# Kernel optimization log

Hardware: AMD Instinct MI355X
Metric: run time of the kernel (lower is better)

## Reference

```python
import jax, jax.numpy as jnp
import numpy as np

R, C, H, W = 500, 512, 38, 38      # rois, VGG channels, feature-map HxW (img 608 / 16)
K, HID, POOL, SCALE = 20, 4096, 3, 16
FEAT = C * POOL * POOL             # 4608, matches fc6 in_features


def setup_inputs():
    key = jax.random.key(0)
    ks = jax.random.split(key, 12)
    fmap = jax.random.normal(ks[0], (C, H, W), dtype=jnp.float32)
    # ROIs in original image coords (x1,y1,x2,y2); width/height >= 48 px so that
    # after /16 + floor every ROI is non-degenerate (none filtered out).
    x1 = jax.random.randint(ks[1], (R,), 0, 288)
    y1 = jax.random.randint(ks[2], (R,), 0, 288)
    bw = jax.random.randint(ks[3], (R,), 48, 304)
    bh = jax.random.randint(ks[4], (R,), 48, 304)
    rois = jnp.stack([x1, y1, x1 + bw, y1 + bh], axis=1).astype(jnp.float32)
    label = jax.random.bernoulli(ks[5], 0.3, (K,)).astype(jnp.float32)
    s = 0.01
    W6 = jax.random.normal(ks[6], (FEAT, HID), jnp.float32) * s
    b6 = jnp.zeros((HID,), jnp.float32)
    W7 = jax.random.normal(ks[7], (HID, HID), jnp.float32) * s
    b7 = jnp.zeros((HID,), jnp.float32)
    W8c = jax.random.normal(ks[8], (HID, K), jnp.float32) * s
    b8c = jnp.zeros((K,), jnp.float32)
    W8d = jax.random.normal(ks[9], (HID, K), jnp.float32) * s
    b8d = jnp.zeros((K,), jnp.float32)
    return dict(fmap=fmap, rois=rois, label=label, W6=W6, b6=b6, W7=W7, b7=b7,
                W8c=W8c, b8c=b8c, W8d=W8d, b8d=b8d)


def _roi_pool(fmap, rois):
    # scaled_rois = origin_rois / 16, sliced as integer indices (floor)
    sc = jnp.floor(rois / SCALE).astype(jnp.int32)          # [R,4]
    x1, y1, x2, y2 = sc[:, 0], sc[:, 1], sc[:, 2], sc[:, 3]

    def binmask(lo, hi, size):
        # adaptive-max-pool bins: [lo + floor(j*L/3), lo + ceil((j+1)*L/3))
        L = hi - lo                                          # [R]
        j = jnp.arange(POOL)
        start = lo[:, None] + (j[None, :] * L[:, None]) // POOL
        end = lo[:, None] + (-((-(j[None, :] + 1) * L[:, None]) // POOL))
        pos = jnp.arange(size)
        return (pos[None, None, :] >= start[:, :, None]) & (pos[None, None, :] < end[:, :, None])

    cm = binmask(x1, x2, W)                                  # [R,3,W]
    rm = binmask(y1, y2, H)                                  # [R,3,H]
    neg = jnp.finfo(fmap.dtype).min
    # max over x within each x-bin: [R,C,H,3]
    tmp = jnp.max(jnp.where(cm[:, None, None, :, :], fmap[None, :, :, None, :], neg), axis=-1)
    # max over y within each y-bin: [R,C,3,3]
    pooled = jnp.max(jnp.where(rm[:, None, :, :, None], tmp[:, :, None, :, :], neg), axis=3)
    return pooled.reshape(R, FEAT), sc.astype(jnp.float32)


def _spatial_reg(scores, fc7, rois_sc, label):
    # faithful to original: argsort ascending, index 0 taken as the reference box,
    # and bboxes_iou interprets (x1,y1,x2,y2) as (x,y,w,h) — replicated as-is.
    idx = jnp.argsort(scores, axis=0)                        # [R,K]

    def per_class(idx_k, s_k, lab_k):
        h, rest = idx_k[0], idx_k[1:]
        hb = rois_sc[h]                                      # [4]
        rb = rois_sc[rest]                                   # [R-1,4]
        b1x2, b1y2 = rb[:, 0] + rb[:, 2], rb[:, 1] + rb[:, 3]
        b2x2, b2y2 = hb[0] + hb[2], hb[1] + hb[3]
        iw = jnp.clip(jnp.minimum(b1x2, b2x2) - jnp.maximum(rb[:, 0], hb[0]) + 1, 0)
        ih = jnp.clip(jnp.minimum(b1y2, b2y2) - jnp.maximum(rb[:, 1], hb[1]) + 1, 0)
        inter = iw * ih
        a1 = (b1x2 - rb[:, 0] + 1) * (b1y2 - rb[:, 1] + 1)
        a2 = (b2x2 - hb[0] + 1) * (b2y2 - hb[1] + 1)
        iou = inter / (a1 + a2 - inter)
        m = (iou > 0.6).astype(fc7.dtype)                    # [R-1]
        rf = fc7[rest] * m[:, None]
        diff = (rf - fc7[h]) * s_k[rest][:, None]
        return lab_k * 0.5 * jnp.sum(diff * diff)

    regs = jax.vmap(per_class)(idx.T, scores.T, label)       # [K]
    return jnp.sum(regs) / K


def reference(fmap, rois, label, W6, b6, W7, b7, W8c, b8c, W8d, b8d):
    feat, rois_sc = _roi_pool(fmap, rois)                    # [R,4608]
    fc6 = feat @ W6 + b6
    fc7 = fc6 @ W7 + b7
    pc = jax.nn.softmax(fc7 @ W8c + b8c, axis=1)             # per-roi over classes
    pd = jax.nn.softmax(fc7 @ W8d + b8d, axis=0)             # per-class over rois
    scores = pc * pd                                         # [R,K]
    out = jnp.sum(scores, axis=0)                            # [K], in (0,1)
    bce = -jnp.mean(label * jnp.log(out) + (1.0 - label) * jnp.log(1.0 - out))
    reg = _spatial_reg(scores, fc7, rois_sc, label)
    return scores, bce + reg, reg
```

## Files before the change

kernel.cpp:

```cpp
#include <hip/hip_runtime.h>
#include <cstdint>
#include <cstddef>

#define DEV __device__ __forceinline__

typedef __bf16 bf16_t;
typedef __bf16 bf16x8 __attribute__((ext_vector_type(8)));
typedef float  f32x4  __attribute__((ext_vector_type(4)));
typedef float  f32x2  __attribute__((ext_vector_type(2)));
typedef unsigned int u32x4 __attribute__((ext_vector_type(4)));

DEV bf16_t f2bf(float x) { return (bf16_t)x; }

constexpr int R_ = 500, C_ = 512, H_ = 38, W_ = 38, K_ = 20;
constexpr int HID = 4096, FEAT = 4608, MP = 512;
constexpr int HW = H_ * W_;

constexpr size_t alup(size_t x) { return (x + 255) & ~(size_t)255; }
constexpr size_t O_FMT  = 0;
constexpr size_t O_RSC  = alup(O_FMT  + (size_t)HW*C_*4);
constexpr size_t O_FEAT = alup(O_RSC  + (size_t)R_*4*4);
constexpr size_t O_FC6  = alup(O_FEAT + (size_t)MP*FEAT*2);
constexpr size_t O_FC7  = alup(O_FC6  + (size_t)MP*HID*2);
constexpr size_t O_PC   = alup(O_FC7  + (size_t)MP*HID*4);
constexpr size_t O_LD   = alup(O_PC   + (size_t)R_*K_*4);
constexpr size_t O_AN   = alup(O_LD   + (size_t)R_*K_*4);
constexpr size_t O_OS   = alup(O_AN   + (size_t)MP*4);
constexpr size_t O_HI   = alup(O_OS   + (size_t)K_*4);
constexpr size_t O_D    = alup(O_HI   + (size_t)K_*4);
constexpr size_t O_W8T  = alup(O_D    + (size_t)R_*K_*4);
constexpr size_t O_PART = alup(O_W8T  + (size_t)2*K_*HID*4);
constexpr size_t WS_K4  = O_PART + (size_t)4*MP*HID*4;

__global__ void __launch_bounds__(256) k_transpose(const float* __restrict__ fmap,
                                                   float* __restrict__ fmapt) {
    __shared__ float tile[32][33];
    int p0 = blockIdx.x * 32, c0 = blockIdx.y * 32;
    int tx = threadIdx.x & 31, ty = threadIdx.x >> 5;
#pragma unroll
    for (int i = 0; i < 4; ++i) {
        int c = c0 + ty + i*8, p = p0 + tx;
        tile[ty + i*8][tx] = (p < HW) ? fmap[(size_t)c*HW + p] : 0.f;
    }
    __syncthreads();
#pragma unroll
    for (int i = 0; i < 4; ++i) {
        int p = p0 + ty + i*8, c = c0 + tx;
        if (p < HW) fmapt[(size_t)p*C_ + c] = tile[tx][ty + i*8];
    }
}

__global__ void __launch_bounds__(256) k_w8t(const float* __restrict__ W8c,
                                             const float* __restrict__ W8d,
                                             float* __restrict__ W8T) {
    int k = blockIdx.x;
    const float* src = (k < K_) ? W8c : W8d;
    int kk = (k < K_) ? k : k - K_;
    for (int i = threadIdx.x; i < HID; i += 256)
        W8T[(size_t)k*HID + i] = src[(size_t)i*K_ + kk];
}

__global__ void __launch_bounds__(256) k_roipool(const float* __restrict__ fmapt,
                                                 const float* __restrict__ rois,
                                                 bf16_t* __restrict__ feat,
                                                 float* __restrict__ rois_sc) {
    int r = blockIdx.x, bin = blockIdx.y, t = threadIdx.x;
    if (r >= R_) {
        feat[(size_t)r*FEAT + (size_t)t*9       + bin] = (bf16_t)0.f;
        feat[(size_t)r*FEAT + (size_t)(t+256)*9 + bin] = (bf16_t)0.f;
        return;
    }
    int x1 = (int)floorf(rois[r*4+0] * 0.0625f);
    int y1 = (int)floorf(rois[r*4+1] * 0.0625f);
    int x2 = (int)floorf(rois[r*4+2] * 0.0625f);
    int y2 = (int)floorf(rois[r*4+3] * 0.0625f);
    if (bin == 0 && t == 0) {
        rois_sc[r*4+0] = (float)x1; rois_sc[r*4+1] = (float)y1;
        rois_sc[r*4+2] = (float)x2; rois_sc[r*4+3] = (float)y2;
    }
    int Lx = x2 - x1, Ly = y2 - y1;
    int pr = bin / 3, px = bin - pr*3;
    int rs = y1 + (pr*Ly)/3, re = y1 + ((pr+1)*Ly + 2)/3;
    int cs = x1 + (px*Lx)/3, ce = x1 + ((px+1)*Lx + 2)/3;
    float m0 = -3.402823466e38f, m1 = -3.402823466e38f;
    for (int y = rs; y < re; ++y) {
        const float* rowp = fmapt + (size_t)(y*W_)*C_;
        for (int x = cs; x < ce; ++x) {
            const float* p = rowp + (size_t)x*C_;
            m0 = fmaxf(m0, p[t]);
            m1 = fmaxf(m1, p[t + 256]);
        }
    }
    feat[(size_t)r*FEAT + (size_t)t*9       + bin] = f2bf(m0);
    feat[(size_t)r*FEAT + (size_t)(t+256)*9 + bin] = f2bf(m1);
}

__global__ void __launch_bounds__(256, 2)
k_gemm(const bf16_t* __restrict__ A, const float* __restrict__ B,
       float* __restrict__ part, int KDIM, int nts) {
    __shared__ bf16_t Asm[2][128*64];
    __shared__ bf16_t Bsm[2][128*64];
    const int t = threadIdx.x;
    const int lane = t & 63, wid = t >> 6;
    const int wr = wid >> 1, wc = wid & 1;

    const int flat = blockIdx.x + 32*blockIdx.y + 128*blockIdx.z;
    const int q = 16 * gridDim.z;
    const int v = (flat & 7) * q + (flat >> 3);
    const int by = v & 3, bx = (v >> 2) & 31, bz = v >> 7;

    const int brow = by * 128, bcol = bx * 128;
    const int kt0 = bz * nts;

    f32x4 acc[4][4] = {};
    f32x2 br[16];
    const int n2 = t & 63, kgl = t >> 6;

    auto stage_A = [&](int kt, int buf) {
        const bf16_t* Ag = A + (size_t)brow*KDIM + kt*64;
#pragma unroll
        for (int i = 0; i < 4; ++i) {
            int s = t + i*256;
            int row = s >> 3;
            int kb = (s & 7) ^ ((row >> 1) & 7);
            const bf16_t* src = Ag + (size_t)row*KDIM + kb*8;
            bf16_t* dst = &Asm[buf][(size_t)(i*256 + (t & ~63)) * 8];
            __builtin_amdgcn_global_load_lds(
                (const __attribute__((address_space(1))) void*)src,
                (__attribute__((address_space(3))) void*)dst, 16, 0, 0);
        }
    };
    auto load_B = [&](int kt) {
        const float* src = B + (size_t)(kt*64 + kgl*16)*HID + bcol + 2*n2;
#pragma unroll
        for (int j = 0; j < 16; ++j)
            br[j] = *reinterpret_cast<const f32x2*>(src + (size_t)j*HID);
    };
    auto write_B = [&](int buf) {
        const int sw = n2 & 7;
        bf16x8 v0, v1;
#pragma unroll
        for (int j = 0; j < 8; ++j) { v0[j] = f2bf(br[j].x); v1[j] = f2bf(br[j+8].x); }
        *reinterpret_cast<u32x4*>(&Bsm[buf][(size_t)((2*n2)*8 + ((kgl*2    ) ^ sw)) * 8]) = *reinterpret_cast<u32x4*>(&v0);
        *reinterpret_cast<u32x4*>(&Bsm[buf][(size_t)((2*n2)*8 + ((kgl*2 + 1) ^ sw)) * 8]) = *reinterpret_cast<u32x4*>(&v1);
#pragma unroll
        for (int j = 0; j < 8; ++j) { v0[j] = f2bf(br[j].y); v1[j] = f2bf(br[j+8].y); }
        *reinterpret_cast<u32x4*>(&Bsm[buf][(size_t)((2*n2+1)*8 + ((kgl*2    ) ^ sw)) * 8]) = *reinterpret_cast<u32x4*>(&v0);
        *reinterpret_cast<u32x4*>(&Bsm[buf][(size_t)((2*n2+1)*8 + ((kgl*2 + 1) ^ sw)) * 8]) = *reinterpret_cast<u32x4*>(&v1);
    };

    stage_A(kt0, 0);
    load_B(kt0);
    write_B(0);
    __syncthreads();

    for (int it = 0; it < nts; ++it) {
        const int cur = it & 1;
        if (it + 1 < nts) { stage_A(kt0 + it + 1, cur ^ 1); load_B(kt0 + it + 1); }
#pragma unroll
        for (int kk = 0; kk < 2; ++kk) {
            const int kb = kk*4 + (lane >> 4);
            bf16x8 af[4], bfr[4];
#pragma unroll
            for (int m = 0; m < 4; ++m) {
                int row = wr*64 + m*16 + (lane & 15);
                af[m] = *reinterpret_cast<const bf16x8*>(
                    &Asm[cur][(size_t)(row*8 + (kb ^ ((row >> 1) & 7))) * 8]);
            }
#pragma unroll
            for (int n = 0; n < 4; ++n) {
                int nn = wc*64 + n*16 + (lane & 15);
                bfr[n] = *reinterpret_cast<const bf16x8*>(
                    &Bsm[cur][(size_t)(nn*8 + (kb ^ ((nn >> 1) & 7))) * 8]);
            }
#pragma unroll
            for (int m = 0; m < 4; ++m)
#pragma unroll
                for (int n = 0; n < 4; ++n)
                    acc[m][n] = __builtin_amdgcn_mfma_f32_16x16x32_bf16(af[m], bfr[n], acc[m][n], 0, 0, 0);
        }
        if (it + 1 < nts) { write_B(cur ^ 1); __syncthreads(); }
    }

    float* dst = part + (size_t)bz * MP * HID;
#pragma unroll
    for (int m = 0; m < 4; ++m) {
        int row0 = brow + wr*64 + m*16 + ((lane >> 4) << 2);
#pragma unroll
        for (int n = 0; n < 4; ++n) {
            int col = bcol + wc*64 + n*16 + (lane & 15);
#pragma unroll
            for (int j = 0; j < 4; ++j)
                dst[(size_t)(row0 + j)*HID + col] = acc[m][n][j];
        }
    }
}

__global__ void __launch_bounds__(256) k_reduce(const float* __restrict__ part,
                                                const float* __restrict__ bias,
                                                bf16_t* __restrict__ ob, float* __restrict__ of,
                                                int ksplit) {
    size_t idx = ((size_t)blockIdx.x*256 + threadIdx.x) * 4;
    f32x4 s = *reinterpret_cast<const f32x4*>(part + idx);
    for (int ss = 1; ss < ksplit; ++ss)
        s += *reinterpret_cast<const f32x4*>(part + (size_t)ss*MP*HID + idx);
    int col = (int)(idx & (HID - 1));
    s += *reinterpret_cast<const f32x4*>(bias + col);
    if (ob) {
#pragma unroll
        for (int j = 0; j < 4; ++j) ob[idx + j] = f2bf(s[j]);
    } else {
        *reinterpret_cast<f32x4*>(of + idx) = s;
    }
}

__global__ void __launch_bounds__(256) k_heads(const float* __restrict__ fc7,
        const float* __restrict__ W8T,
        const float* __restrict__ b8c, const float* __restrict__ b8d,
        float* __restrict__ pc, float* __restrict__ ld_out, float* __restrict__ An) {
    int r = blockIdx.x, t = threadIdx.x;
    float ac[20] = {}, ad[20] = {}, aa = 0.f;
    const float* frow = fc7 + (size_t)r*HID;
    for (int e = 0; e < 16; ++e) {
        int i = e*256 + t;
        float x = frow[i];
        aa = fmaf(x, x, aa);
#pragma unroll
        for (int k = 0; k < 20; ++k) {
            ac[k] = fmaf(x, W8T[(size_t)k*HID + i], ac[k]);
            ad[k] = fmaf(x, W8T[(size_t)(K_ + k)*HID + i], ad[k]);
        }
    }
#pragma unroll
    for (int k = 0; k < 20; ++k)
        for (int off = 1; off < 64; off <<= 1) {
            ac[k] += __shfl_xor(ac[k], off, 64);
            ad[k] += __shfl_xor(ad[k], off, 64);
        }
    for (int off = 1; off < 64; off <<= 1) aa += __shfl_xor(aa, off, 64);

    __shared__ float red[4][41];
    int wid = t >> 6, lane = t & 63;
    if (lane == 0) {
#pragma unroll
        for (int k = 0; k < 20; ++k) { red[wid][k] = ac[k]; red[wid][20+k] = ad[k]; }
        red[wid][40] = aa;
    }
    __syncthreads();
    __shared__ float lcs[20];
    if (t < 41) {
        float v = red[0][t] + red[1][t] + red[2][t] + red[3][t];
        if (t < 20)      lcs[t] = v + b8c[t];
        else if (t < 40) ld_out[r*K_ + (t-20)] = v + b8d[t-20];
        else             An[r] = v;
    }
    __syncthreads();
    if (t == 0) {
        float mx = lcs[0];
#pragma unroll
        for (int k = 1; k < 20; ++k) mx = fmaxf(mx, lcs[k]);
        float s = 0.f, e[20];
#pragma unroll
        for (int k = 0; k < 20; ++k) { e[k] = expf(lcs[k] - mx); s += e[k]; }
        float inv = 1.f / s;
#pragma unroll
        for (int k = 0; k < 20; ++k) pc[r*K_ + k] = e[k] * inv;
    }
}

__global__ void __launch_bounds__(256) k_pd(const float* __restrict__ ld,
        const float* __restrict__ pc, float* __restrict__ scores,
        float* __restrict__ out_sum, int* __restrict__ h_idx) {
    int k = blockIdx.x, t = threadIdx.x;
    __shared__ float sh[4];
    float m = -3.402823466e38f;
    for (int r = t; r < R_; r += 256) m = fmaxf(m, ld[r*K_ + k]);
    for (int off = 1; off < 64; off <<= 1) m = fmaxf(m, __shfl_xor(m, off, 64));
    if ((t & 63) == 0) sh[t >> 6] = m;
    __syncthreads();
    m = fmaxf(fmaxf(sh[0], sh[1]), fmaxf(sh[2], sh[3]));
    __syncthreads();
    float s = 0.f;
    for (int r = t; r < R_; r += 256) s += expf(ld[r*K_ + k] - m);
    for (int off = 1; off < 64; off <<= 1) s += __shfl_xor(s, off, 64);
    if ((t & 63) == 0) sh[t >> 6] = s;
    __syncthreads();
    s = sh[0] + sh[1] + sh[2] + sh[3];
    float inv = 1.f / s;

    float osum = 0.f, bv = 3.402823466e38f; int bi = 0x7fffffff;
    for (int r = t; r < R_; r += 256) {
        float p  = expf(ld[r*K_ + k] - m) * inv;
        float sc = pc[r*K_ + k] * p;
        scores[r*K_ + k] = sc;
        osum += sc;
        if (sc < bv || (sc == bv && r < bi)) { bv = sc; bi = r; }
    }
    for (int off = 1; off < 64; off <<= 1) osum += __shfl_xor(osum, off, 64);
    for (int off = 1; off < 64; off <<= 1) {
        float v2 = __shfl_xor(bv, off, 64);
        int   i2 = __shfl_xor(bi, off, 64);
        if (v2 < bv || (v2 == bv && i2 < bi)) { bv = v2; bi = i2; }
    }
    __shared__ float so[4], mv[4]; __shared__ int mi[4];
    if ((t & 63) == 0) { so[t >> 6] = osum; mv[t >> 6] = bv; mi[t >> 6] = bi; }
    __syncthreads();
    if (t == 0) {
        out_sum[k] = so[0] + so[1] + so[2] + so[3];
        float v = mv[0]; int i = mi[0];
        for (int w = 1; w < 4; ++w)
            if (mv[w] < v || (mv[w] == v && mi[w] < i)) { v = mv[w]; i = mi[w]; }
        h_idx[k] = i;
    }
}

__global__ void __launch_bounds__(256) k_dmat(const float* __restrict__ fc7,
        const int* __restrict__ h_idx, float* __restrict__ D) {
    int r = blockIdx.x, t = threadIdx.x;
    const float* frow = fc7 + (size_t)r*HID;
    const float* hrow[20];
#pragma unroll
    for (int k = 0; k < 20; ++k) hrow[k] = fc7 + (size_t)h_idx[k]*HID;
    float acc[20] = {};
    for (int e = 0; e < 16; ++e) {
        int i = e*256 + t;
        float x = frow[i];
#pragma unroll
        for (int k = 0; k < 20; ++k) acc[k] = fmaf(x, hrow[k][i], acc[k]);
    }
#pragma unroll
    for (int k = 0; k < 20; ++k)
        for (int off = 1; off < 64; off <<= 1) acc[k] += __shfl_xor(acc[k], off, 64);
    __shared__ float red[4][20];
    int wid = t >> 6, lane = t & 63;
    if (lane == 0) {
#pragma unroll
        for (int k = 0; k < 20; ++k) red[wid][k] = acc[k];
    }
    __syncthreads();
    if (t < 20) D[r*K_ + t] = red[0][t] + red[1][t] + red[2][t] + red[3][t];
}

__global__ void __launch_bounds__(256) k_final(const float* __restrict__ out_sum,
        const int* __restrict__ h_idx, const float* __restrict__ label,
        const float* __restrict__ scores, const float* __restrict__ D,
        const float* __restrict__ An, const float* __restrict__ rois_sc,
        float* __restrict__ dout) {
    int t = threadIdx.x;
    __shared__ float bsh[20];
    if (t < 20) {
        float o = out_sum[t], lab = label[t];
        bsh[t] = lab * logf(o) + (1.f - lab) * logf(1.f - o);
    }
    __syncthreads();

    float rp = 0.f;
    for (int i = t; i < R_*K_; i += 256) {
        int r = i / 20, k = i - r*20;
        int h = h_idx[k];
        if (r == h) continue;
        float lab = label[k];
        if (lab == 0.f) continue;
        float s = scores[r*K_ + k];
        const float* rb = rois_sc + r*4;
        const float* hb = rois_sc + h*4;
        float b1x2 = rb[0] + rb[2], b1y2 = rb[1] + rb[3];
        float b2x2 = hb[0] + hb[2], b2y2 = hb[1] + hb[3];
        float iw = fmaxf(fminf(b1x2, b2x2) - fmaxf(rb[0], hb[0]) + 1.f, 0.f);
        float ih = fmaxf(fminf(b1y2, b2y2) - fmaxf(rb[1], hb[1]) + 1.f, 0.f);
        float inter = iw * ih;
        float a1 = (b1x2 - rb[0] + 1.f) * (b1y2 - rb[1] + 1.f);
        float a2 = (b2x2 - hb[0] + 1.f) * (b2y2 - hb[1] + 1.f);
        float iou = inter / (a1 + a2 - inter);
        float mm = (iou > 0.6f) ? 1.f : 0.f;
        float term = mm * (An[r] - 2.f * D[r*K_ + k]) + An[h];
        rp += lab * 0.5f * s * s * term;
    }
    for (int off = 1; off < 64; off <<= 1) rp += __shfl_xor(rp, off, 64);
    __shared__ float rsh[4];
    if ((t & 63) == 0) rsh[t >> 6] = rp;
    __syncthreads();
    if (t == 0) {
        float reg = (rsh[0] + rsh[1] + rsh[2] + rsh[3]) / (float)K_;
        float b = 0.f;
        for (int k = 0; k < 20; ++k) b += bsh[k];
        float bce = -b / (float)K_;
        dout[R_*K_]     = bce + reg;
        dout[R_*K_ + 1] = reg;
    }
}

extern "C" void kernel_launch(void* const* d_in, const int* in_sizes, int n_in,
                              void* d_out, int out_size, void* d_ws, size_t ws_size,
                              hipStream_t stream) {
    const float* fmap  = (const float*)d_in[0];
    const float* rois  = (const float*)d_in[1];
    const float* label = (const float*)d_in[2];
    const float* W6    = (const float*)d_in[3];
    const float* b6    = (const float*)d_in[4];
    const float* W7    = (const float*)d_in[5];
    const float* b7    = (const float*)d_in[6];
    const float* W8c   = (const float*)d_in[7];
    const float* b8c   = (const float*)d_in[8];
    const float* W8d   = (const float*)d_in[9];
    const float* b8d   = (const float*)d_in[10];
    char* ws = (char*)d_ws;
    float* out = (float*)d_out;

    float*  fmapt = (float*)(ws + O_FMT);
    float*  roisc = (float*)(ws + O_RSC);
    bf16_t* feat  = (bf16_t*)(ws + O_FEAT);
    bf16_t* fc6   = (bf16_t*)(ws + O_FC6);
    float*  fc7   = (float*)(ws + O_FC7);
    float*  pc    = (float*)(ws + O_PC);
    float*  ld    = (float*)(ws + O_LD);
    float*  An    = (float*)(ws + O_AN);
    float*  osum  = (float*)(ws + O_OS);
    int*    hidx  = (int*)(ws + O_HI);
    float*  Dm    = (float*)(ws + O_D);
    float*  w8t   = (float*)(ws + O_W8T);
    float*  part  = (float*)(ws + O_PART);

    const int ksplit = 4;

    k_transpose<<<dim3((HW + 31)/32, C_/32), dim3(256), 0, stream>>>(fmap, fmapt);
    k_w8t      <<<dim3(2*K_),   dim3(256), 0, stream>>>(W8c, W8d, w8t);
    k_roipool  <<<dim3(MP, 9),  dim3(256), 0, stream>>>(fmapt, rois, feat, roisc);

    k_gemm  <<<dim3(HID/128, MP/128, ksplit), dim3(256), 0, stream>>>(feat, W6, part, FEAT, (FEAT/64)/ksplit);
    k_reduce<<<dim3((MP*HID)/1024), dim3(256), 0, stream>>>(part, b6, fc6, (float*)nullptr, ksplit);

    k_gemm  <<<dim3(HID/128, MP/128, ksplit), dim3(256), 0, stream>>>(fc6, W7, part, HID, (HID/64)/ksplit);
    k_reduce<<<dim3((MP*HID)/1024), dim3(256), 0, stream>>>(part, b7, (bf16_t*)nullptr, fc7, ksplit);

    k_heads<<<dim3(R_), dim3(256), 0, stream>>>(fc7, w8t, b8c, b8d, pc, ld, An);
    k_pd   <<<dim3(K_), dim3(256), 0, stream>>>(ld, pc, out, osum, hidx);
    k_dmat <<<dim3(R_), dim3(256), 0, stream>>>(fc7, hidx, Dm);
    k_final<<<dim3(1),  dim3(256), 0, stream>>>(osum, hidx, label, out, Dm, An, roisc, out);
}
```

Baseline: 180.5 us.

## Narrow GEMM tiles to 128x64 and split head/dmat dot products over K

The fc6/fc7 GEMM now uses 128x64 output tiles, which doubles the block count and cuts B shared memory so three blocks can fit per CU. The per-ROI head and D-matrix kernels are replaced by a K-split k_dotcols kernel that stages weight columns in LDS and reuses them across 64 rows, followed by small reduction kernels. This targets low parallelism and repeated global weight reads in the heads, at the cost of extra partial-sum traffic, two more launches, and less A-tile reuse in the GEMM.

```diff
diff --git a/kernel.cpp b/kernel.cpp
--- a/kernel.cpp
+++ b/kernel.cpp
@@ -30,7 +30,8 @@
 constexpr size_t O_D    = alup(O_HI   + (size_t)K_*4);
 constexpr size_t O_W8T  = alup(O_D    + (size_t)R_*K_*4);
 constexpr size_t O_PART = alup(O_W8T  + (size_t)2*K_*HID*4);
-constexpr size_t WS_K4  = O_PART + (size_t)4*MP*HID*4;
+constexpr size_t O_HP   = O_PART;
+constexpr size_t O_DP   = O_PART + (size_t)4*1024*1024;
 
 __global__ void __launch_bounds__(256) k_transpose(const float* __restrict__ fmap,
                                                    float* __restrict__ fmapt) {
@@ -95,26 +96,25 @@
     feat[(size_t)r*FEAT + (size_t)(t+256)*9 + bin] = f2bf(m1);
 }
 
-__global__ void __launch_bounds__(256, 2)
+__global__ void __launch_bounds__(256, 3)
 k_gemm(const bf16_t* __restrict__ A, const float* __restrict__ B,
        float* __restrict__ part, int KDIM, int nts) {
     __shared__ bf16_t Asm[2][128*64];
-    __shared__ bf16_t Bsm[2][128*64];
+    __shared__ bf16_t Bsm[2][64*64];
     const int t = threadIdx.x;
     const int lane = t & 63, wid = t >> 6;
     const int wr = wid >> 1, wc = wid & 1;
 
-    const int flat = blockIdx.x + 32*blockIdx.y + 128*blockIdx.z;
-    const int q = 16 * gridDim.z;
-    const int v = (flat & 7) * q + (flat >> 3);
-    const int by = v & 3, bx = (v >> 2) & 31, bz = v >> 7;
-
-    const int brow = by * 128, bcol = bx * 128;
+    const int flat = blockIdx.x + 64*blockIdx.y + 256*blockIdx.z;
+    const int v = (flat & 7) * 128 + (flat >> 3);
+    const int by = v & 3, bx = (v >> 2) & 63, bz = v >> 8;
+
+    const int brow = by * 128, bcol = bx * 64;
     const int kt0 = bz * nts;
 
-    f32x4 acc[4][4] = {};
-    f32x2 br[16];
-    const int n2 = t & 63, kgl = t >> 6;
+    f32x4 acc[4][2] = {};
+    f32x2 br[8];
+    const int n2 = t & 31, kgl = t >> 5;
 
     auto stage_A = [&](int kt, int buf) {
         const bf16_t* Ag = A + (size_t)brow*KDIM + kt*64;
@@ -131,22 +131,18 @@
         }
     };
     auto load_B = [&](int kt) {
-        const float* src = B + (size_t)(kt*64 + kgl*16)*HID + bcol + 2*n2;
-#pragma unroll
-        for (int j = 0; j < 16; ++j)
+        const float* src = B + (size_t)(kt*64 + kgl*8)*HID + bcol + 2*n2;
+#pragma unroll
+        for (int j = 0; j < 8; ++j)
             br[j] = *reinterpret_cast<const f32x2*>(src + (size_t)j*HID);
     };
     auto write_B = [&](int buf) {
         const int sw = n2 & 7;
         bf16x8 v0, v1;
 #pragma unroll
-        for (int j = 0; j < 8; ++j) { v0[j] = f2bf(br[j].x); v1[j] = f2bf(br[j+8].x); }
-        *reinterpret_cast<u32x4*>(&Bsm[buf][(size_t)((2*n2)*8 + ((kgl*2    ) ^ sw)) * 8]) = *reinterpret_cast<u32x4*>(&v0);
-        *reinterpret_cast<u32x4*>(&Bsm[buf][(size_t)((2*n2)*8 + ((kgl*2 + 1) ^ sw)) * 8]) = *reinterpret_cast<u32x4*>(&v1);
-#pragma unroll
-        for (int j = 0; j < 8; ++j) { v0[j] = f2bf(br[j].y); v1[j] = f2bf(br[j+8].y); }
-        *reinterpret_cast<u32x4*>(&Bsm[buf][(size_t)((2*n2+1)*8 + ((kgl*2    ) ^ sw)) * 8]) = *reinterpret_cast<u32x4*>(&v0);
-        *reinterpret_cast<u32x4*>(&Bsm[buf][(size_t)((2*n2+1)*8 + ((kgl*2 + 1) ^ sw)) * 8]) = *reinterpret_cast<u32x4*>(&v1);
+        for (int j = 0; j < 8; ++j) { v0[j] = f2bf(br[j].x); v1[j] = f2bf(br[j].y); }
+        *reinterpret_cast<u32x4*>(&Bsm[buf][(size_t)((2*n2    )*8 + (kgl ^ sw)) * 8]) = *reinterpret_cast<u32x4*>(&v0);
+        *reinterpret_cast<u32x4*>(&Bsm[buf][(size_t)((2*n2 + 1)*8 + (kgl ^ sw)) * 8]) = *reinterpret_cast<u32x4*>(&v1);
     };
 
     stage_A(kt0, 0);
@@ -160,7 +156,7 @@
 #pragma unroll
         for (int kk = 0; kk < 2; ++kk) {
             const int kb = kk*4 + (lane >> 4);
-            bf16x8 af[4], bfr[4];
+            bf16x8 af[4], bfr[2];
 #pragma unroll
             for (int m = 0; m < 4; ++m) {
                 int row = wr*64 + m*16 + (lane & 15);
@@ -168,15 +164,15 @@
                     &Asm[cur][(size_t)(row*8 + (kb ^ ((row >> 1) & 7))) * 8]);
             }
 #pragma unroll
-            for (int n = 0; n < 4; ++n) {
-                int nn = wc*64 + n*16 + (lane & 15);
+            for (int n = 0; n < 2; ++n) {
+                int nn = wc*32 + n*16 + (lane & 15);
                 bfr[n] = *reinterpret_cast<const bf16x8*>(
                     &Bsm[cur][(size_t)(nn*8 + (kb ^ ((nn >> 1) & 7))) * 8]);
             }
 #pragma unroll
             for (int m = 0; m < 4; ++m)
 #pragma unroll
-                for (int n = 0; n < 4; ++n)
+                for (int n = 0; n < 2; ++n)
                     acc[m][n] = __builtin_amdgcn_mfma_f32_16x16x32_bf16(af[m], bfr[n], acc[m][n], 0, 0, 0);
         }
         if (it + 1 < nts) { write_B(cur ^ 1); __syncthreads(); }
@@ -187,8 +183,8 @@
     for (int m = 0; m < 4; ++m) {
         int row0 = brow + wr*64 + m*16 + ((lane >> 4) << 2);
 #pragma unroll
-        for (int n = 0; n < 4; ++n) {
-            int col = bcol + wc*64 + n*16 + (lane & 15);
+        for (int n = 0; n < 2; ++n) {
+            int col = bcol + wc*32 + n*16 + (lane & 15);
 #pragma unroll
             for (int j = 0; j < 4; ++j)
                 dst[(size_t)(row0 + j)*HID + col] = acc[m][n][j];
@@ -214,57 +210,102 @@
     }
 }
 
-__global__ void __launch_bounds__(256) k_heads(const float* __restrict__ fc7,
-        const float* __restrict__ W8T,
+template<int NOUT, bool SELF>
+__global__ void __launch_bounds__(256) k_dotcols(const float* __restrict__ fc7,
+        const float* __restrict__ Bmat, const int* __restrict__ bidx,
+        float* __restrict__ partial) {
+    constexpr int NO = NOUT + (SELF ? 1 : 0);
+    constexpr int SLICE = NOUT*16 + 4;
+    __shared__ float Bs[8 * SLICE];
+    const int rb = blockIdx.x, kb = blockIdx.y, t = threadIdx.x;
+    const int k0 = kb * 128;
+    for (int i = t; i < NOUT*32; i += 256) {
+        int o = i >> 5, c = i & 31;
+        const float* src = bidx ? fc7 + (size_t)bidx[o]*HID : Bmat + (size_t)o*HID;
+        f32x4 v = *reinterpret_cast<const f32x4*>(src + k0 + c*4);
+        *reinterpret_cast<f32x4*>(&Bs[(c >> 2)*SLICE + o*16 + (c & 3)*4]) = v;
+    }
+    __syncthreads();
+    const int lane = t & 63, w = t >> 6;
+    const int ri = lane >> 3, kk = lane & 7;
+    const int r0 = rb*64 + w*16 + ri*2;
+    f32x4 x0[4], x1[4];
+    const float* f0 = fc7 + (size_t)r0*HID + k0 + kk*16;
+#pragma unroll
+    for (int j = 0; j < 4; ++j) {
+        x0[j] = *reinterpret_cast<const f32x4*>(f0 + j*4);
+        x1[j] = *reinterpret_cast<const f32x4*>(f0 + HID + j*4);
+    }
+    float acc0[NO], acc1[NO];
+#pragma unroll
+    for (int o = 0; o < NOUT; ++o) {
+        f32x4 s0 = {}, s1 = {};
+#pragma unroll
+        for (int j = 0; j < 4; ++j) {
+            f32x4 wv = *reinterpret_cast<const f32x4*>(&Bs[kk*SLICE + o*16 + j*4]);
+            s0 += x0[j] * wv;
+            s1 += x1[j] * wv;
+        }
+        acc0[o] = s0[0]+s0[1]+s0[2]+s0[3];
+        acc1[o] = s1[0]+s1[1]+s1[2]+s1[3];
+    }
+    if (SELF) {
+        f32x4 s0 = {}, s1 = {};
+#pragma unroll
+        for (int j = 0; j < 4; ++j) { s0 += x0[j]*x0[j]; s1 += x1[j]*x1[j]; }
+        acc0[NO-1] = s0[0]+s0[1]+s0[2]+s0[3];
+        acc1[NO-1] = s1[0]+s1[1]+s1[2]+s1[3];
+    }
+#pragma unroll
+    for (int o = 0; o < NO; ++o) {
+#pragma unroll
+        for (int m = 1; m < 8; m <<= 1) {
+            acc0[o] += __shfl_xor(acc0[o], m, 64);
+            acc1[o] += __shfl_xor(acc1[o], m, 64);
+        }
+    }
+    if (kk == 0) {
+#pragma unroll
+        for (int o = 0; o < NO; ++o) {
+            partial[((size_t)kb*MP + r0    )*NO + o] = acc0[o];
+            partial[((size_t)kb*MP + r0 + 1)*NO + o] = acc1[o];
+        }
+    }
+}
+
+__global__ void __launch_bounds__(64) k_headred(const float* __restrict__ hpart,
         const float* __restrict__ b8c, const float* __restrict__ b8d,
-        float* __restrict__ pc, float* __restrict__ ld_out, float* __restrict__ An) {
+        float* __restrict__ pc, float* __restrict__ ld, float* __restrict__ An) {
     int r = blockIdx.x, t = threadIdx.x;
-    float ac[20] = {}, ad[20] = {}, aa = 0.f;
-    const float* frow = fc7 + (size_t)r*HID;
-    for (int e = 0; e < 16; ++e) {
-        int i = e*256 + t;
-        float x = frow[i];
-        aa = fmaf(x, x, aa);
-#pragma unroll
-        for (int k = 0; k < 20; ++k) {
-            ac[k] = fmaf(x, W8T[(size_t)k*HID + i], ac[k]);
-            ad[k] = fmaf(x, W8T[(size_t)(K_ + k)*HID + i], ad[k]);
-        }
-    }
-#pragma unroll
-    for (int k = 0; k < 20; ++k)
-        for (int off = 1; off < 64; off <<= 1) {
-            ac[k] += __shfl_xor(ac[k], off, 64);
-            ad[k] += __shfl_xor(ad[k], off, 64);
-        }
-    for (int off = 1; off < 64; off <<= 1) aa += __shfl_xor(aa, off, 64);
-
-    __shared__ float red[4][41];
-    int wid = t >> 6, lane = t & 63;
-    if (lane == 0) {
-#pragma unroll
-        for (int k = 0; k < 20; ++k) { red[wid][k] = ac[k]; red[wid][20+k] = ad[k]; }
-        red[wid][40] = aa;
-    }
-    __syncthreads();
     __shared__ float lcs[20];
     if (t < 41) {
-        float v = red[0][t] + red[1][t] + red[2][t] + red[3][t];
-        if (t < 20)      lcs[t] = v + b8c[t];
-        else if (t < 40) ld_out[r*K_ + (t-20)] = v + b8d[t-20];
-        else             An[r] = v;
+        float s = 0.f;
+        for (int kb = 0; kb < 32; ++kb) s += hpart[((size_t)kb*MP + r)*41 + t];
+        if (t < 20)      lcs[t] = s + b8c[t];
+        else if (t < 40) ld[r*K_ + (t-20)] = s + b8d[t-20];
+        else             An[r] = s;
     }
     __syncthreads();
     if (t == 0) {
         float mx = lcs[0];
 #pragma unroll
         for (int k = 1; k < 20; ++k) mx = fmaxf(mx, lcs[k]);
-        float s = 0.f, e[20];
-#pragma unroll
-        for (int k = 0; k < 20; ++k) { e[k] = expf(lcs[k] - mx); s += e[k]; }
-        float inv = 1.f / s;
+        float sum = 0.f, e[20];
+#pragma unroll
+        for (int k = 0; k < 20; ++k) { e[k] = expf(lcs[k] - mx); sum += e[k]; }
+        float inv = 1.f / sum;
 #pragma unroll
         for (int k = 0; k < 20; ++k) pc[r*K_ + k] = e[k] * inv;
+    }
+}
+
+__global__ void __launch_bounds__(64) k_dmatred(const float* __restrict__ dpart,
+                                                float* __restrict__ D) {
+    int r = blockIdx.x, t = threadIdx.x;
+    if (t < 20) {
+        float s = 0.f;
+        for (int kb = 0; kb < 32; ++kb) s += dpart[((size_t)kb*MP + r)*20 + t];
+        D[r*K_ + t] = s;
     }
 }
 
@@ -312,33 +353,6 @@
             if (mv[w] < v || (mv[w] == v && mi[w] < i)) { v = mv[w]; i = mi[w]; }
         h_idx[k] = i;
     }
-}
-
-__global__ void __launch_bounds__(256) k_dmat(const float* __restrict__ fc7,
-        const int* __restrict__ h_idx, float* __restrict__ D) {
-    int r = blockIdx.x, t = threadIdx.x;
-    const float* frow = fc7 + (size_t)r*HID;
-    const float* hrow[20];
-#pragma unroll
-    for (int k = 0; k < 20; ++k) hrow[k] = fc7 + (size_t)h_idx[k]*HID;
-    float acc[20] = {};
-    for (int e = 0; e < 16; ++e) {
-        int i = e*256 + t;
-        float x = frow[i];
-#pragma unroll
-        for (int k = 0; k < 20; ++k) acc[k] = fmaf(x, hrow[k][i], acc[k]);
-    }
-#pragma unroll
-    for (int k = 0; k < 20; ++k)
-        for (int off = 1; off < 64; off <<= 1) acc[k] += __shfl_xor(acc[k], off, 64);
-    __shared__ float red[4][20];
-    int wid = t >> 6, lane = t & 63;
-    if (lane == 0) {
-#pragma unroll
-        for (int k = 0; k < 20; ++k) red[wid][k] = acc[k];
-    }
-    __syncthreads();
-    if (t < 20) D[r*K_ + t] = red[0][t] + red[1][t] + red[2][t] + red[3][t];
 }
 
 __global__ void __launch_bounds__(256) k_final(const float* __restrict__ out_sum,
@@ -420,6 +434,8 @@
     float*  Dm    = (float*)(ws + O_D);
     float*  w8t   = (float*)(ws + O_W8T);
     float*  part  = (float*)(ws + O_PART);
+    float*  hpart = (float*)(ws + O_HP);
+    float*  dpart = (float*)(ws + O_DP);
 
     const int ksplit = 4;
 
@@ -427,14 +443,16 @@
     k_w8t      <<<dim3(2*K_),   dim3(256), 0, stream>>>(W8c, W8d, w8t);
     k_roipool  <<<dim3(MP, 9),  dim3(256), 0, stream>>>(fmapt, rois, feat, roisc);
 
-    k_gemm  <<<dim3(HID/128, MP/128, ksplit), dim3(256), 0, stream>>>(feat, W6, part, FEAT, (FEAT/64)/ksplit);
+    k_gemm  <<<dim3(HID/64, MP/128, ksplit), dim3(256), 0, stream>>>(feat, W6, part, FEAT, (FEAT/64)/ksplit);
     k_reduce<<<dim3((MP*HID)/1024), dim3(256), 0, stream>>>(part, b6, fc6, (float*)nullptr, ksplit);
 
-    k_gemm  <<<dim3(HID/128, MP/128, ksplit), dim3(256), 0, stream>>>(fc6, W7, part, HID, (HID/64)/ksplit);
+    k_gemm  <<<dim3(HID/64, MP/128, ksplit), dim3(256), 0, stream>>>(fc6, W7, part, HID, (HID/64)/ksplit);
     k_reduce<<<dim3((MP*HID)/1024), dim3(256), 0, stream>>>(part, b7, (bf16_t*)nullptr, fc7, ksplit);
 
-    k_heads<<<dim3(R_), dim3(256), 0, stream>>>(fc7, w8t, b8c, b8d, pc, ld, An);
-    k_pd   <<<dim3(K_), dim3(256), 0, stream>>>(ld, pc, out, osum, hidx);
-    k_dmat <<<dim3(R_), dim3(256), 0, stream>>>(fc7, hidx, Dm);
-    k_final<<<dim3(1),  dim3(256), 0, stream>>>(osum, hidx, label, out, Dm, An, roisc, out);
-}
+    k_dotcols<40, true><<<dim3(MP/64, HID/128), dim3(256), 0, stream>>>(fc7, w8t, (const int*)nullptr, hpart);
+    k_headred<<<dim3(R_), dim3(64), 0, stream>>>(hpart, b8c, b8d, pc, ld, An);
+    k_pd     <<<dim3(K_), dim3(256), 0, stream>>>(ld, pc, out, osum, hidx);
+    k_dotcols<20, false><<<dim3(MP/64, HID/128), dim3(256), 0, stream>>>(fc7, (const float*)nullptr, hidx, dpart);
+    k_dmatred<<<dim3(R_), dim3(64), 0, stream>>>(dpart, Dm);
+    k_final  <<<dim3(1),  dim3(256), 0, stream>>>(osum, hidx, label, out, Dm, An, roisc, out);
+}
```

After: 199.1 us. 10.3% more time.
